# Kernel optimization log

Hardware: AMD Instinct MI355X
Metric: run time of the kernel (lower is better)

The kernel has to match this reference:

```python
import jax, jax.numpy as jnp
import numpy as np

H = 256; B = 64; MAXF = 32; L = 50; S = 50
TAU = 1.0; BIAS = 0.0  # m_tau / m_bias (undefined in source; fixed constants)


def setup_inputs() -> dict:
    key = jax.random.key(0)
    ks = jax.random.split(key, 16)
    s = 1.0 / np.sqrt(H)
    return {
        "self_x": jax.random.normal(ks[0], (B, H), jnp.float32),
        "common_x": jax.random.normal(ks[1], (B, MAXF, S, H), jnp.float32),
        "common_time": jax.random.uniform(ks[2], (B, MAXF, S), jnp.float32),
        "friend_x": jax.random.normal(ks[3], (B, MAXF, L, H), jnp.float32),
        "Wih0": jax.random.normal(ks[4], (3 * H, H), jnp.float32) * s,
        "Whh0": jax.random.normal(ks[5], (3 * H, H), jnp.float32) * s,
        "bih0": jax.random.normal(ks[6], (3 * H,), jnp.float32) * s,
        "bhh0": jax.random.normal(ks[7], (3 * H,), jnp.float32) * s,
        "Wih1": jax.random.normal(ks[8], (3 * H, H), jnp.float32) * s,
        "Whh1": jax.random.normal(ks[9], (3 * H, H), jnp.float32) * s,
        "bih1": jax.random.normal(ks[10], (3 * H,), jnp.float32) * s,
        "bhh1": jax.random.normal(ks[11], (3 * H,), jnp.float32) * s,
        "Wf": jax.random.normal(ks[12], (H, 2 * H), jnp.float32) * s,   # m_linear_friend
        "Wb": jax.random.normal(ks[13], (H, H), jnp.float32) * s,       # m_linear_beta
        "friend_len": jax.random.randint(ks[14], (B, MAXF), 1, L + 1, jnp.int32),
        "friend_num": jax.random.randint(ks[15], (B,), 1, MAXF + 1, jnp.int32),
        "common_len": jax.random.randint(jax.random.fold_in(key, 99), (B, MAXF), 1, S + 1, jnp.int32),
    }


def _gru_layer(x, Wih, Whh, bih, bhh):
    # x: [N, L, H] -> outputs [N, L, H]; torch GRU gate math, zero init hidden
    def step(h, xt):
        gi = xt @ Wih.T + bih
        gh = h @ Whh.T + bhh
        ir, iz, inn = jnp.split(gi, 3, axis=-1)
        hr, hz, hn = jnp.split(gh, 3, axis=-1)
        r = jax.nn.sigmoid(ir + hr)
        z = jax.nn.sigmoid(iz + hz)
        n = jnp.tanh(inn + r * hn)
        h = (1.0 - z) * n + z * h
        return h, h
    h0 = jnp.zeros((x.shape[0], Whh.shape[1]), x.dtype)
    _, ys = jax.lax.scan(step, h0, jnp.swapaxes(x, 0, 1))
    return jnp.swapaxes(ys, 0, 1)


def reference(self_x, common_x, common_time, friend_x,
              Wih0, Whh0, bih0, bhh0, Wih1, Whh1, bih1, bhh1,
              Wf, Wb, friend_len, friend_num, common_len):
    # --- GRU over all (user, friend) sequences, flattened ---
    fx = friend_x.reshape(B * MAXF, L, H)
    fx = _gru_layer(fx, Wih0, Whh0, bih0, bhh0)
    fx = _gru_layer(fx, Wih1, Whh1, bih1, bhh1)
    fx = fx.reshape(B, MAXF, L, H)

    # mask invalid time steps, gather last valid hidden state per friend
    t_mask = (jnp.arange(L)[None, None, :] < friend_len[:, :, None])  # [B,MAXF,L]
    fx = fx * t_mask[..., None].astype(fx.dtype)
    last_idx = jnp.clip(friend_len - 1, 0, L - 1)
    friend_last = jnp.take_along_axis(fx, last_idx[:, :, None, None], axis=2)[:, :, 0, :]  # [B,MAXF,H]

    # repeat_interleave(self_x) equivalent in dense layout, concat, project
    self_rep = jnp.broadcast_to(self_x[:, None, :], (B, MAXF, H))
    sf = jnp.concatenate([self_rep, friend_last], axis=-1)  # [B,MAXF,2H]
    sf = jnp.einsum('bfk,hk->bfh', sf, Wf)                   # m_linear_friend

    # attention scores over common items: bmm + softplus
    proj_c = jnp.einsum('bfsh,gh->bfsg', common_x, Wb)       # m_linear_beta, g==H
    scores = jax.nn.softplus(jnp.einsum('bfsh,bfh->bfs', proj_c, sf))

    temporal = jnp.exp(-common_time / TAU + BIAS)
    c_mask = (jnp.arange(S)[None, None, :] < common_len[:, :, None]).astype(scores.dtype)
    tf = jnp.sum(scores * temporal * c_mask, axis=-1)        # [B,MAXF]

    # pad_sequence semantics: invalid friend slots are zero (logits and vectors)
    f_valid = (jnp.arange(MAXF)[None, :] < friend_num[:, None]).astype(tf.dtype)
    tf = tf * f_valid
    friend_last = friend_last * f_valid[..., None]

    w = jax.nn.softmax(tf, axis=-1)                          # over padded MAXF, as in source
    return jnp.sum(w[..., None] * friend_last, axis=1)       # [B,H]
```

## Files before the change

kernel.cpp:

```cpp
#include <hip/hip_runtime.h>
#include <hip/hip_bf16.h>
#include <stdint.h>

#define HD    256
#define LL    50
#define SS    50
#define NB    64
#define MAXF  32
#define NSEQ  2048
#define MB    32
#define NBLK  64
#define XP    264

typedef __attribute__((ext_vector_type(8)))  short bf16x8;
typedef __attribute__((ext_vector_type(16))) float f32x16;
typedef __attribute__((ext_vector_type(4)))  unsigned short u16x4;

__device__ __forceinline__ f32x16 mfma32(bf16x8 a, bf16x8 b, f32x16 c) {
    return __builtin_amdgcn_mfma_f32_32x32x16_bf16(a, b, c, 0, 0, 0);
}

__device__ __forceinline__ unsigned short f2bf_rne(float f) {
    union { float f; uint32_t u; } v; v.f = f;
    uint32_t u = v.u;
    uint32_t r = u + 0x7FFFu + ((u >> 16) & 1u);
    return (unsigned short)(r >> 16);
}
__device__ __forceinline__ float bf2f(unsigned short b) {
    union { float f; uint32_t u; } v; v.u = ((uint32_t)b) << 16;
    return v.f;
}

__global__ void pack_kernel(const float* __restrict__ Wih0, const float* __restrict__ Whh0,
                            const float* __restrict__ Wih1, const float* __restrict__ Whh1,
                            const float* __restrict__ Wf,
                            unsigned short* __restrict__ wpk,
                            float* __restrict__ WfT) {
    int idx = blockIdx.x * blockDim.x + threadIdx.x;
    const int TOTW = 1572864;
    if (idx < TOTW) {
        int j    = idx & 7;
        int lane = (idx >> 3) & 63;
        int fr   = (idx >> 9) % 12;
        int t2   = (idx >> 9) / 12;
        int ks   = t2 & 15;
        int m    = (t2 >> 4) & 1;
        int l    = (t2 >> 5) & 1;
        int wvv  = t2 >> 6;
        int gate = fr >> 2, sub = (fr >> 1) & 1, plane = fr & 1;
        const float* W = (l == 0) ? (m == 0 ? Wih0 : Whh0)
                                  : (m == 0 ? Wih1 : Whh1);
        int n = gate * 256 + wvv * 64 + sub * 32 + (lane & 31);
        int k = ks * 16 + (lane >> 5) * 8 + j;
        float v = W[n * HD + k];
        unsigned short hi = f2bf_rne(v);
        wpk[idx] = plane ? f2bf_rne(v - bf2f(hi)) : hi;
    } else {
        int idx2 = idx - TOTW;
        if (idx2 < 512 * 256) {
            int k = idx2 >> 8; int h = idx2 & 255;
            WfT[k * 256 + h] = Wf[h * 512 + k];
        }
    }
}

__global__ void sort_kernel(const int* __restrict__ flen, int* __restrict__ sid) {
    __shared__ int hist[64];
    __shared__ int offs[64];
    int tid = threadIdx.x;
    if (tid < 64) hist[tid] = 0;
    __syncthreads();
    for (int i = tid; i < NSEQ; i += blockDim.x) atomicAdd(&hist[flen[i]], 1);
    __syncthreads();
    if (tid == 0) {
        int acc = 0;
        for (int v = 1; v <= 50; v++) { offs[v] = acc; acc += hist[v]; }
    }
    __syncthreads();
    for (int i = tid; i < NSEQ; i += blockDim.x) {
        int pos = atomicAdd(&offs[flen[i]], 1);
        sid[pos] = i;
    }
}

__global__ __launch_bounds__(256) __attribute__((amdgpu_waves_per_eu(1, 1)))
void gru_kernel(const float* __restrict__ friend_x,
                const int* __restrict__ flen,
                const int* __restrict__ sid,
                const unsigned short* __restrict__ wpk,
                const float* __restrict__ bih0, const float* __restrict__ bhh0,
                const float* __restrict__ bih1, const float* __restrict__ bhh1,
                float* __restrict__ friend_last) {
    __shared__ __align__(16) unsigned short Xhi[MB][XP],  Xlo[MB][XP];
    __shared__ __align__(16) unsigned short H0hi[MB][XP], H0lo[MB][XP];
    __shared__ __align__(16) unsigned short H1hi[MB][XP], H1lo[MB][XP];
    __shared__ int sidS[MB], lenS[MB];

    const int tid  = threadIdx.x;
    const int g    = blockIdx.x;
    const int wv   = tid >> 6;
    const int lane = tid & 63;
    const int l31  = lane & 31;
    const int half = lane >> 5;

    if (tid < MB) {
        int s_ = sid[g * MB + tid];
        sidS[tid] = s_;
        lenS[tid] = flen[s_];
    }
    for (int i = tid; i < MB * XP / 2; i += 256) {
        ((uint32_t*)&H0hi[0][0])[i] = 0; ((uint32_t*)&H0lo[0][0])[i] = 0;
        ((uint32_t*)&H1hi[0][0])[i] = 0; ((uint32_t*)&H1lo[0][0])[i] = 0;
    }
    __syncthreads();

    int maxlen = 0;
#pragma unroll
    for (int s = 0; s < MB; s++) maxlen = max(maxlen, lenS[s]);

    const int j0 = wv * 64 + l31;

    float b0R[2], b0Z[2], b0Ni[2], b0Nh[2];
    float b1R[2], b1Z[2], b1Ni[2], b1Nh[2];
#pragma unroll
    for (int sub = 0; sub < 2; sub++) {
        int j = j0 + 32 * sub;
        b0R[sub]  = bih0[j] + bhh0[j];
        b0Z[sub]  = bih0[256 + j] + bhh0[256 + j];
        b0Ni[sub] = bih0[512 + j];
        b0Nh[sub] = bhh0[512 + j];
        b1R[sub]  = bih1[j] + bhh1[j];
        b1Z[sub]  = bih1[256 + j] + bhh1[256 + j];
        b1Ni[sub] = bih1[512 + j];
        b1Nh[sub] = bhh1[512 + j];
    }

    int srow[8];
#pragma unroll
    for (int r = 0; r < 8; r++) srow[r] = sidS[wv * 8 + r];

    float h0c[2][16], h1c[2][16];
#pragma unroll
    for (int sub = 0; sub < 2; sub++)
#pragma unroll
        for (int rg = 0; rg < 16; rg++) { h0c[sub][rg] = 0.f; h1c[sub][rg] = 0.f; }

    const int fragBase = l31 * XP + half * 8;

    auto loadB12 = [&](bf16x8* B, const unsigned short* p) {
#pragma unroll
        for (int f = 0; f < 12; f++) B[f] = *(const bf16x8*)(p + f * 512);
    };

    auto compute9 = [&](const bf16x8* B, bf16x8 ah, bf16x8 al,
                        f32x16* aR, f32x16* aZ, f32x16* aN) {
#pragma unroll
        for (int sub = 0; sub < 2; sub++) {
            aR[sub] = mfma32(ah, B[sub * 2],     aR[sub]);
            aR[sub] = mfma32(al, B[sub * 2],     aR[sub]);
            aR[sub] = mfma32(ah, B[sub * 2 + 1], aR[sub]);
            aZ[sub] = mfma32(ah, B[4 + sub * 2],     aZ[sub]);
            aZ[sub] = mfma32(al, B[4 + sub * 2],     aZ[sub]);
            aZ[sub] = mfma32(ah, B[4 + sub * 2 + 1], aZ[sub]);
            aN[sub] = mfma32(ah, B[8 + sub * 2],     aN[sub]);
            aN[sub] = mfma32(al, B[8 + sub * 2],     aN[sub]);
            aN[sub] = mfma32(ah, B[8 + sub * 2 + 1], aN[sub]);
        }
    };

    auto halfMM = [&](const unsigned short* pm,
                      const unsigned short* Ah_, const unsigned short* Al_,
                      f32x16* aR, f32x16* aZ, f32x16* aN) {
        bf16x8 B0[12], B1[12], ah0, al0, ah1, al1;
        loadB12(B0, pm);
        ah0 = *(const bf16x8*)(Ah_ + fragBase);
        al0 = *(const bf16x8*)(Al_ + fragBase);
        loadB12(B1, pm + 6144);
        ah1 = *(const bf16x8*)(Ah_ + fragBase + 16);
        al1 = *(const bf16x8*)(Al_ + fragBase + 16);
#pragma unroll 1
        for (int ks = 0; ks < 16; ks += 2) {
            compute9(B0, ah0, al0, aR, aZ, aN);
            if (ks + 2 < 16) {
                loadB12(B0, pm + (size_t)(ks + 2) * 6144);
                ah0 = *(const bf16x8*)(Ah_ + fragBase + (ks + 2) * 16);
                al0 = *(const bf16x8*)(Al_ + fragBase + (ks + 2) * 16);
            }
            compute9(B1, ah1, al1, aR, aZ, aN);
            if (ks + 3 < 16) {
                loadB12(B1, pm + (size_t)(ks + 3) * 6144);
                ah1 = *(const bf16x8*)(Ah_ + fragBase + (ks + 3) * 16);
                al1 = *(const bf16x8*)(Al_ + fragBase + (ks + 3) * 16);
            }
        }
    };

    auto initAcc = [&](f32x16* a, const float* b) {
#pragma unroll
        for (int sub = 0; sub < 2; sub++) {
            f32x16 v;
#pragma unroll
            for (int i = 0; i < 16; i++) v[i] = b[sub];
            a[sub] = v;
        }
    };

    auto epi = [&](f32x16* aR, f32x16* aZ, f32x16* aNi, f32x16* aNh,
                   float (*hc)[16],
                   unsigned short (*Ohi)[XP], unsigned short (*Olo)[XP],
                   bool gather, int t) {
#pragma unroll
        for (int sub = 0; sub < 2; sub++) {
            const int j = j0 + 32 * sub;
#pragma unroll
            for (int rg = 0; rg < 16; rg++) {
                const int row = (rg & 3) + ((rg >> 2) << 3) + (half << 2);
                float rr = 1.f / (1.f + __expf(-aR[sub][rg]));
                float zz = 1.f / (1.f + __expf(-aZ[sub][rg]));
                float nx = aNi[sub][rg] + rr * aNh[sub][rg];
                float e  = __expf(-2.f * fabsf(nx));
                float th = 1.f - 2.f * e / (1.f + e);
                th = (nx < 0.f) ? -th : th;
                float hNew = (1.f - zz) * th + zz * hc[sub][rg];
                hc[sub][rg] = hNew;
                unsigned short hi_ = f2bf_rne(hNew);
                Ohi[row][j] = hi_;
                Olo[row][j] = f2bf_rne(hNew - bf2f(hi_));
                if (gather && t == lenS[row] - 1)
                    friend_last[(size_t)sidS[row] * HD + j] = hNew;
            }
        }
    };

    auto stageWrite = [&](const float4* sx) {
#pragma unroll
        for (int r = 0; r < 8; r++) {
            int row = wv * 8 + r;
            float vals[4] = { sx[r].x, sx[r].y, sx[r].z, sx[r].w };
            u16x4 hi4, lo4;
#pragma unroll
            for (int e2 = 0; e2 < 4; e2++) {
                unsigned short h_ = f2bf_rne(vals[e2]);
                hi4[e2] = h_;
                lo4[e2] = f2bf_rne(vals[e2] - bf2f(h_));
            }
            *(u16x4*)&Xhi[row][lane * 4] = hi4;
            *(u16x4*)&Xlo[row][lane * 4] = lo4;
        }
    };

    {
        float4 sx[8];
#pragma unroll
        for (int r = 0; r < 8; r++)
            sx[r] = ((const float4*)(friend_x + ((size_t)srow[r] * LL) * HD))[lane];
        stageWrite(sx);
    }
    __syncthreads();

    const unsigned short* pw0 = wpk + (size_t)(wv * 2 + 0) * 196608 + (size_t)lane * 8;
    const unsigned short* pw1 = wpk + (size_t)(wv * 2 + 1) * 196608 + (size_t)lane * 8;

    for (int t = 0; t < maxlen; t++) {
        int tn = (t + 1 < maxlen) ? t + 1 : t;
        float4 sx[8];
#pragma unroll
        for (int r = 0; r < 8; r++)
            sx[r] = ((const float4*)(friend_x + ((size_t)srow[r] * LL + tn) * HD))[lane];

        f32x16 aR[2], aZ[2], aNi[2], aNh[2];
        initAcc(aR, b0R); initAcc(aZ, b0Z); initAcc(aNi, b0Ni); initAcc(aNh, b0Nh);
        halfMM(pw0,         &Xhi[0][0],  &Xlo[0][0],  aR, aZ, aNi);
        halfMM(pw0 + 98304, &H0hi[0][0], &H0lo[0][0], aR, aZ, aNh);
        __syncthreads();
        epi(aR, aZ, aNi, aNh, h0c, H0hi, H0lo, false, t);
        stageWrite(sx);
        __syncthreads();
        initAcc(aR, b1R); initAcc(aZ, b1Z); initAcc(aNi, b1Ni); initAcc(aNh, b1Nh);
        halfMM(pw1,         &H0hi[0][0], &H0lo[0][0], aR, aZ, aNi);
        halfMM(pw1 + 98304, &H1hi[0][0], &H1lo[0][0], aR, aZ, aNh);
        __syncthreads();
        epi(aR, aZ, aNi, aNh, h1c, H1hi, H1lo, true, t);
    }
}

__global__ __launch_bounds__(256)
void sfv_kernel(const float* __restrict__ self_x, const float* __restrict__ fl,
                const float* __restrict__ WfT, const float* __restrict__ Wb,
                float* __restrict__ vout) {
    __shared__ float S[256];
    __shared__ float T[256][33];
    int b = blockIdx.x, tid = threadIdx.x;
    S[tid] = self_x[b * 256 + tid];
    for (int i = tid; i < 32 * 256; i += 256) {
        int f = i >> 8, k = i & 255;
        T[k][f] = fl[((size_t)(b * 32 + f)) * 256 + k];
    }
    __syncthreads();
    float acc0 = 0.f;
    for (int k = 0; k < 256; k++) acc0 += WfT[k * 256 + tid] * S[k];
    float acc[32];
#pragma unroll
    for (int f = 0; f < 32; f++) acc[f] = acc0;
    for (int k = 0; k < 256; k++) {
        float w = WfT[(256 + k) * 256 + tid];
#pragma unroll
        for (int f = 0; f < 32; f++) acc[f] += w * T[k][f];
    }
    __syncthreads();
#pragma unroll
    for (int f = 0; f < 32; f++) T[tid][f] = acc[f];
    __syncthreads();
    float av[32];
#pragma unroll
    for (int f = 0; f < 32; f++) av[f] = 0.f;
    for (int gg = 0; gg < 256; gg++) {
        float w = Wb[gg * 256 + tid];
#pragma unroll
        for (int f = 0; f < 32; f++) av[f] += w * T[gg][f];
    }
#pragma unroll
    for (int f = 0; f < 32; f++)
        vout[((size_t)(b * 32 + f)) * 256 + tid] = av[f];
}

__global__ __launch_bounds__(256)
void tf_kernel(const float* __restrict__ common_x, const float* __restrict__ common_time,
               const int* __restrict__ clen, const float* __restrict__ v,
               float* __restrict__ tf) {
    __shared__ float V[256];
    __shared__ float partial[4];
    int n = blockIdx.x, tid = threadIdx.x, wv = tid >> 6, lane = tid & 63;
    V[tid] = v[(size_t)n * 256 + tid];
    __syncthreads();
    float4 vv = ((const float4*)V)[lane];
    int cl = clen[n];
    float acc = 0.f;
    for (int s = wv; s < SS; s += 4) {
        float4 cx = ((const float4*)(common_x + ((size_t)n * SS + s) * HD))[lane];
        float d = cx.x * vv.x + cx.y * vv.y + cx.z * vv.z + cx.w * vv.w;
#pragma unroll
        for (int off = 32; off; off >>= 1) d += __shfl_xor(d, off);
        if (lane == 0 && s < cl) {
            float sp = (d > 20.f) ? d : log1pf(__expf(d));
            acc += sp * __expf(-common_time[n * SS + s]);
        }
    }
    if (lane == 0) partial[wv] = acc;
    __syncthreads();
    if (tid == 0) tf[n] = partial[0] + partial[1] + partial[2] + partial[3];
}

__global__ __launch_bounds__(256)
void out_kernel(const float* __restrict__ tf, const int* __restrict__ fnum,
                const float* __restrict__ fl, float* __restrict__ out) {
    __shared__ float e[32];
    __shared__ float tfm[32];
    __shared__ float Zs;
    int b = blockIdx.x, tid = threadIdx.x;
    int nv = fnum[b];
    if (tid < 32) tfm[tid] = (tid < nv) ? tf[b * 32 + tid] : 0.f;
    __syncthreads();
    if (tid == 0) {
        float m = tfm[0];
        for (int f = 1; f < 32; f++) m = fmaxf(m, tfm[f]);
        float Z = 0.f;
        for (int f = 0; f < 32; f++) { e[f] = __expf(tfm[f] - m); Z += e[f]; }
        Zs = Z;
    }
    __syncthreads();
    float Zi = 1.f / Zs;
    float o = 0.f;
    for (int f = 0; f < nv; f++)
        o += e[f] * Zi * fl[((size_t)(b * 32 + f)) * 256 + tid];
    out[b * 256 + tid] = o;
}

extern "C" void kernel_launch(void* const* d_in, const int* in_sizes, int n_in,
                              void* d_out, int out_size, void* d_ws, size_t ws_size,
                              hipStream_t stream) {
    (void)in_sizes; (void)n_in; (void)out_size; (void)ws_size;
    const float* self_x      = (const float*)d_in[0];
    const float* common_x    = (const float*)d_in[1];
    const float* common_time = (const float*)d_in[2];
    const float* friend_x    = (const float*)d_in[3];
    const float* Wih0 = (const float*)d_in[4];
    const float* Whh0 = (const float*)d_in[5];
    const float* bih0 = (const float*)d_in[6];
    const float* bhh0 = (const float*)d_in[7];
    const float* Wih1 = (const float*)d_in[8];
    const float* Whh1 = (const float*)d_in[9];
    const float* bih1 = (const float*)d_in[10];
    const float* bhh1 = (const float*)d_in[11];
    const float* Wf   = (const float*)d_in[12];
    const float* Wb   = (const float*)d_in[13];
    const int* flen   = (const int*)d_in[14];
    const int* fnum   = (const int*)d_in[15];
    const int* clen   = (const int*)d_in[16];
    float* out = (float*)d_out;

    char* ws = (char*)d_ws;
    unsigned short* wpk = (unsigned short*)ws; ws += (size_t)1572864 * 2;
    float* WfT = (float*)ws;  ws += (size_t)512 * 256 * 4;
    int*   sid = (int*)ws;    ws += (size_t)2048 * 4;
    float* fl  = (float*)ws;  ws += (size_t)2048 * 256 * 4;
    float* vv  = (float*)ws;  ws += (size_t)2048 * 256 * 4;
    float* tf  = (float*)ws;  ws += (size_t)2048 * 4;

    pack_kernel<<<6656, 256, 0, stream>>>(Wih0, Whh0, Wih1, Whh1, Wf, wpk, WfT);
    sort_kernel<<<1, 256, 0, stream>>>(flen, sid);
    gru_kernel<<<NBLK, 256, 0, stream>>>(friend_x, flen, sid, wpk,
                                         bih0, bhh0, bih1, bhh1, fl);
    sfv_kernel<<<64, 256, 0, stream>>>(self_x, fl, WfT, Wb, vv);
    tf_kernel<<<2048, 256, 0, stream>>>(common_x, common_time, clen, vv, tf);
    out_kernel<<<64, 256, 0, stream>>>(tf, fnum, fl, out);
}
```

Baseline: 2.760 ms.

## Split GRU hidden columns across 8 waves per block instead of 4

```diff
diff --git a/kernel.cpp b/kernel.cpp
--- a/kernel.cpp
+++ b/kernel.cpp
@@ -41,16 +41,16 @@
     if (idx < TOTW) {
         int j    = idx & 7;
         int lane = (idx >> 3) & 63;
-        int fr   = (idx >> 9) % 12;
-        int t2   = (idx >> 9) / 12;
+        int fr   = (idx >> 9) % 6;
+        int t2   = (idx >> 9) / 6;
         int ks   = t2 & 15;
         int m    = (t2 >> 4) & 1;
         int l    = (t2 >> 5) & 1;
         int wvv  = t2 >> 6;
-        int gate = fr >> 2, sub = (fr >> 1) & 1, plane = fr & 1;
+        int gate = fr >> 1, plane = fr & 1;
         const float* W = (l == 0) ? (m == 0 ? Wih0 : Whh0)
                                   : (m == 0 ? Wih1 : Whh1);
-        int n = gate * 256 + wvv * 64 + sub * 32 + (lane & 31);
+        int n = gate * 256 + wvv * 32 + (lane & 31);
         int k = ks * 16 + (lane >> 5) * 8 + j;
         float v = W[n * HD + k];
         unsigned short hi = f2bf_rne(v);
@@ -83,7 +83,7 @@
     }
 }
 
-__global__ __launch_bounds__(256) __attribute__((amdgpu_waves_per_eu(1, 1)))
+__global__ __launch_bounds__(512) __attribute__((amdgpu_waves_per_eu(2)))
 void gru_kernel(const float* __restrict__ friend_x,
                 const int* __restrict__ flen,
                 const int* __restrict__ sid,
@@ -108,7 +108,7 @@
         sidS[tid] = s_;
         lenS[tid] = flen[s_];
     }
-    for (int i = tid; i < MB * XP / 2; i += 256) {
+    for (int i = tid; i < MB * XP / 2; i += 512) {
         ((uint32_t*)&H0hi[0][0])[i] = 0; ((uint32_t*)&H0lo[0][0])[i] = 0;
         ((uint32_t*)&H1hi[0][0])[i] = 0; ((uint32_t*)&H1lo[0][0])[i] = 0;
     }
@@ -118,124 +118,110 @@
 #pragma unroll
     for (int s = 0; s < MB; s++) maxlen = max(maxlen, lenS[s]);
 
-    const int j0 = wv * 64 + l31;
-
-    float b0R[2], b0Z[2], b0Ni[2], b0Nh[2];
-    float b1R[2], b1Z[2], b1Ni[2], b1Nh[2];
-#pragma unroll
-    for (int sub = 0; sub < 2; sub++) {
-        int j = j0 + 32 * sub;
-        b0R[sub]  = bih0[j] + bhh0[j];
-        b0Z[sub]  = bih0[256 + j] + bhh0[256 + j];
-        b0Ni[sub] = bih0[512 + j];
-        b0Nh[sub] = bhh0[512 + j];
-        b1R[sub]  = bih1[j] + bhh1[j];
-        b1Z[sub]  = bih1[256 + j] + bhh1[256 + j];
-        b1Ni[sub] = bih1[512 + j];
-        b1Nh[sub] = bhh1[512 + j];
-    }
-
-    int srow[8];
-#pragma unroll
-    for (int r = 0; r < 8; r++) srow[r] = sidS[wv * 8 + r];
-
-    float h0c[2][16], h1c[2][16];
-#pragma unroll
-    for (int sub = 0; sub < 2; sub++)
-#pragma unroll
-        for (int rg = 0; rg < 16; rg++) { h0c[sub][rg] = 0.f; h1c[sub][rg] = 0.f; }
+    const int j0 = wv * 32 + l31;
+
+    float b0R  = bih0[j0] + bhh0[j0];
+    float b0Z  = bih0[256 + j0] + bhh0[256 + j0];
+    float b0Ni = bih0[512 + j0];
+    float b0Nh = bhh0[512 + j0];
+    float b1R  = bih1[j0] + bhh1[j0];
+    float b1Z  = bih1[256 + j0] + bhh1[256 + j0];
+    float b1Ni = bih1[512 + j0];
+    float b1Nh = bhh1[512 + j0];
+
+    int srow[4];
+#pragma unroll
+    for (int r = 0; r < 4; r++) srow[r] = sidS[wv * 4 + r];
 
     const int fragBase = l31 * XP + half * 8;
 
-    auto loadB12 = [&](bf16x8* B, const unsigned short* p) {
-#pragma unroll
-        for (int f = 0; f < 12; f++) B[f] = *(const bf16x8*)(p + f * 512);
+    auto loadB6 = [&](bf16x8* B, const unsigned short* p) {
+#pragma unroll
+        for (int f = 0; f < 6; f++) B[f] = *(const bf16x8*)(p + f * 512);
     };
 
     auto compute9 = [&](const bf16x8* B, bf16x8 ah, bf16x8 al,
-                        f32x16* aR, f32x16* aZ, f32x16* aN) {
-#pragma unroll
-        for (int sub = 0; sub < 2; sub++) {
-            aR[sub] = mfma32(ah, B[sub * 2],     aR[sub]);
-            aR[sub] = mfma32(al, B[sub * 2],     aR[sub]);
-            aR[sub] = mfma32(ah, B[sub * 2 + 1], aR[sub]);
-            aZ[sub] = mfma32(ah, B[4 + sub * 2],     aZ[sub]);
-            aZ[sub] = mfma32(al, B[4 + sub * 2],     aZ[sub]);
-            aZ[sub] = mfma32(ah, B[4 + sub * 2 + 1], aZ[sub]);
-            aN[sub] = mfma32(ah, B[8 + sub * 2],     aN[sub]);
-            aN[sub] = mfma32(al, B[8 + sub * 2],     aN[sub]);
-            aN[sub] = mfma32(ah, B[8 + sub * 2 + 1], aN[sub]);
-        }
+                        f32x16& aRs, f32x16& aZs, f32x16& aNs) {
+        aRs = mfma32(ah, B[0], aRs);
+        aRs = mfma32(al, B[0], aRs);
+        aRs = mfma32(ah, B[1], aRs);
+        aZs = mfma32(ah, B[2], aZs);
+        aZs = mfma32(al, B[2], aZs);
+        aZs = mfma32(ah, B[3], aZs);
+        aNs = mfma32(ah, B[4], aNs);
+        aNs = mfma32(al, B[4], aNs);
+        aNs = mfma32(ah, B[5], aNs);
     };
 
     auto halfMM = [&](const unsigned short* pm,
                       const unsigned short* Ah_, const unsigned short* Al_,
-                      f32x16* aR, f32x16* aZ, f32x16* aN) {
-        bf16x8 B0[12], B1[12], ah0, al0, ah1, al1;
-        loadB12(B0, pm);
-        ah0 = *(const bf16x8*)(Ah_ + fragBase);
-        al0 = *(const bf16x8*)(Al_ + fragBase);
-        loadB12(B1, pm + 6144);
-        ah1 = *(const bf16x8*)(Ah_ + fragBase + 16);
-        al1 = *(const bf16x8*)(Al_ + fragBase + 16);
-#pragma unroll 1
-        for (int ks = 0; ks < 16; ks += 2) {
-            compute9(B0, ah0, al0, aR, aZ, aN);
-            if (ks + 2 < 16) {
-                loadB12(B0, pm + (size_t)(ks + 2) * 6144);
-                ah0 = *(const bf16x8*)(Ah_ + fragBase + (ks + 2) * 16);
-                al0 = *(const bf16x8*)(Al_ + fragBase + (ks + 2) * 16);
+                      f32x16& aRs, f32x16& aZs, f32x16& aNs) {
+        bf16x8 B0[6], B1[6], B2[6], B3[6];
+        loadB6(B0, pm);
+        loadB6(B1, pm + 3072);
+        loadB6(B2, pm + 6144);
+        loadB6(B3, pm + 9216);
+        bf16x8 ahA = *(const bf16x8*)(Ah_ + fragBase);
+        bf16x8 alA = *(const bf16x8*)(Al_ + fragBase);
+        bf16x8 ahB, alB;
+#pragma unroll
+        for (int base = 0; base < 16; base += 4) {
+            ahB = *(const bf16x8*)(Ah_ + fragBase + (base + 1) * 16);
+            alB = *(const bf16x8*)(Al_ + fragBase + (base + 1) * 16);
+            compute9(B0, ahA, alA, aRs, aZs, aNs);
+            if (base + 4 < 16) loadB6(B0, pm + (size_t)(base + 4) * 3072);
+            ahA = *(const bf16x8*)(Ah_ + fragBase + (base + 2) * 16);
+            alA = *(const bf16x8*)(Al_ + fragBase + (base + 2) * 16);
+            compute9(B1, ahB, alB, aRs, aZs, aNs);
+            if (base + 5 < 16) loadB6(B1, pm + (size_t)(base + 5) * 3072);
+            ahB = *(const bf16x8*)(Ah_ + fragBase + (base + 3) * 16);
+            alB = *(const bf16x8*)(Al_ + fragBase + (base + 3) * 16);
+            compute9(B2, ahA, alA, aRs, aZs, aNs);
+            if (base + 6 < 16) loadB6(B2, pm + (size_t)(base + 6) * 3072);
+            {
+                const int kn = (base + 4 < 16) ? base + 4 : 15;
+                ahA = *(const bf16x8*)(Ah_ + fragBase + kn * 16);
+                alA = *(const bf16x8*)(Al_ + fragBase + kn * 16);
             }
-            compute9(B1, ah1, al1, aR, aZ, aN);
-            if (ks + 3 < 16) {
-                loadB12(B1, pm + (size_t)(ks + 3) * 6144);
-                ah1 = *(const bf16x8*)(Ah_ + fragBase + (ks + 3) * 16);
-                al1 = *(const bf16x8*)(Al_ + fragBase + (ks + 3) * 16);
-            }
+            compute9(B3, ahB, alB, aRs, aZs, aNs);
+            if (base + 7 < 16) loadB6(B3, pm + (size_t)(base + 7) * 3072);
         }
     };
 
-    auto initAcc = [&](f32x16* a, const float* b) {
-#pragma unroll
-        for (int sub = 0; sub < 2; sub++) {
-            f32x16 v;
-#pragma unroll
-            for (int i = 0; i < 16; i++) v[i] = b[sub];
-            a[sub] = v;
-        }
-    };
-
-    auto epi = [&](f32x16* aR, f32x16* aZ, f32x16* aNi, f32x16* aNh,
-                   float (*hc)[16],
+    auto initAcc = [&](f32x16& a, float b) {
+        f32x16 v;
+#pragma unroll
+        for (int i = 0; i < 16; i++) v[i] = b;
+        a = v;
+    };
+
+    auto epi = [&](f32x16& aRs, f32x16& aZs, f32x16& aNis, f32x16& aNhs,
                    unsigned short (*Ohi)[XP], unsigned short (*Olo)[XP],
                    bool gather, int t) {
-#pragma unroll
-        for (int sub = 0; sub < 2; sub++) {
-            const int j = j0 + 32 * sub;
-#pragma unroll
-            for (int rg = 0; rg < 16; rg++) {
-                const int row = (rg & 3) + ((rg >> 2) << 3) + (half << 2);
-                float rr = 1.f / (1.f + __expf(-aR[sub][rg]));
-                float zz = 1.f / (1.f + __expf(-aZ[sub][rg]));
-                float nx = aNi[sub][rg] + rr * aNh[sub][rg];
-                float e  = __expf(-2.f * fabsf(nx));
-                float th = 1.f - 2.f * e / (1.f + e);
-                th = (nx < 0.f) ? -th : th;
-                float hNew = (1.f - zz) * th + zz * hc[sub][rg];
-                hc[sub][rg] = hNew;
-                unsigned short hi_ = f2bf_rne(hNew);
-                Ohi[row][j] = hi_;
-                Olo[row][j] = f2bf_rne(hNew - bf2f(hi_));
-                if (gather && t == lenS[row] - 1)
-                    friend_last[(size_t)sidS[row] * HD + j] = hNew;
-            }
+        const int j = j0;
+#pragma unroll
+        for (int rg = 0; rg < 16; rg++) {
+            const int row = (rg & 3) + ((rg >> 2) << 3) + (half << 2);
+            float hOld = bf2f(Ohi[row][j]) + bf2f(Olo[row][j]);
+            float rr = 1.f / (1.f + __expf(-aRs[rg]));
+            float zz = 1.f / (1.f + __expf(-aZs[rg]));
+            float nx = aNis[rg] + rr * aNhs[rg];
+            float e  = __expf(-2.f * fabsf(nx));
+            float th = 1.f - 2.f * e / (1.f + e);
+            th = (nx < 0.f) ? -th : th;
+            float hNew = (1.f - zz) * th + zz * hOld;
+            unsigned short hi_ = f2bf_rne(hNew);
+            Ohi[row][j] = hi_;
+            Olo[row][j] = f2bf_rne(hNew - bf2f(hi_));
+            if (gather && t == lenS[row] - 1)
+                friend_last[(size_t)sidS[row] * HD + j] = hNew;
         }
     };
 
     auto stageWrite = [&](const float4* sx) {
 #pragma unroll
-        for (int r = 0; r < 8; r++) {
-            int row = wv * 8 + r;
+        for (int r = 0; r < 4; r++) {
+            int row = wv * 4 + r;
             float vals[4] = { sx[r].x, sx[r].y, sx[r].z, sx[r].w };
             u16x4 hi4, lo4;
 #pragma unroll
@@ -250,37 +236,38 @@
     };
 
     {
-        float4 sx[8];
-#pragma unroll
-        for (int r = 0; r < 8; r++)
+        float4 sx[4];
+#pragma unroll
+        for (int r = 0; r < 4; r++)
             sx[r] = ((const float4*)(friend_x + ((size_t)srow[r] * LL) * HD))[lane];
         stageWrite(sx);
     }
     __syncthreads();
 
-    const unsigned short* pw0 = wpk + (size_t)(wv * 2 + 0) * 196608 + (size_t)lane * 8;
-    const unsigned short* pw1 = wpk + (size_t)(wv * 2 + 1) * 196608 + (size_t)lane * 8;
-
+    const unsigned short* pw0 = wpk + (size_t)(wv * 2 + 0) * 98304 + (size_t)lane * 8;
+    const unsigned short* pw1 = wpk + (size_t)(wv * 2 + 1) * 98304 + (size_t)lane * 8;
+
+#pragma unroll 1
     for (int t = 0; t < maxlen; t++) {
         int tn = (t + 1 < maxlen) ? t + 1 : t;
-        float4 sx[8];
-#pragma unroll
-        for (int r = 0; r < 8; r++)
+        float4 sx[4];
+#pragma unroll
+        for (int r = 0; r < 4; r++)
             sx[r] = ((const float4*)(friend_x + ((size_t)srow[r] * LL + tn) * HD))[lane];
 
-        f32x16 aR[2], aZ[2], aNi[2], aNh[2];
+        f32x16 aR, aZ, aNi, aNh;
         initAcc(aR, b0R); initAcc(aZ, b0Z); initAcc(aNi, b0Ni); initAcc(aNh, b0Nh);
         halfMM(pw0,         &Xhi[0][0],  &Xlo[0][0],  aR, aZ, aNi);
-        halfMM(pw0 + 98304, &H0hi[0][0], &H0lo[0][0], aR, aZ, aNh);
+        halfMM(pw0 + 49152, &H0hi[0][0], &H0lo[0][0], aR, aZ, aNh);
         __syncthreads();
-        epi(aR, aZ, aNi, aNh, h0c, H0hi, H0lo, false, t);
+        epi(aR, aZ, aNi, aNh, H0hi, H0lo, false, t);
         stageWrite(sx);
         __syncthreads();
         initAcc(aR, b1R); initAcc(aZ, b1Z); initAcc(aNi, b1Ni); initAcc(aNh, b1Nh);
         halfMM(pw1,         &H0hi[0][0], &H0lo[0][0], aR, aZ, aNi);
-        halfMM(pw1 + 98304, &H1hi[0][0], &H1lo[0][0], aR, aZ, aNh);
+        halfMM(pw1 + 49152, &H1hi[0][0], &H1lo[0][0], aR, aZ, aNh);
         __syncthreads();
-        epi(aR, aZ, aNi, aNh, h1c, H1hi, H1lo, true, t);
+        epi(aR, aZ, aNi, aNh, H1hi, H1lo, true, t);
     }
 }
 
@@ -409,7 +396,7 @@
 
     pack_kernel<<<6656, 256, 0, stream>>>(Wih0, Whh0, Wih1, Whh1, Wf, wpk, WfT);
     sort_kernel<<<1, 256, 0, stream>>>(flen, sid);
-    gru_kernel<<<NBLK, 256, 0, stream>>>(friend_x, flen, sid, wpk,
+    gru_kernel<<<NBLK, 512, 0, stream>>>(friend_x, flen, sid, wpk,
                                          bih0, bhh0, bih1, bhh1, fl);
     sfv_kernel<<<64, 256, 0, stream>>>(self_x, fl, WfT, Wb, vv);
     tf_kernel<<<2048, 256, 0, stream>>>(common_x, common_time, clen, vv, tf);
```

Measured after the change: 6.587 ms. 139% more time.
